# Performance work log

Measured on AMD Instinct MI355X. Metric: run time of the kernel, lower is better.

The kernel has to match this reference:

```python
import jax, jax.numpy as jnp
import numpy as np

B, S, ENC_UNITS, DEC_UNITS, NUM_UNITS = 64, 2048, 512, 512, 512


def setup_inputs() -> dict:
    key = jax.random.key(0)
    k_h, k_eo, k_w1, k_b1, k_w2, k_b2, k_v, k_bv = jax.random.split(key, 8)
    sd = 0.05
    return {
        "H": jax.random.normal(k_h, (B, DEC_UNITS), dtype=jnp.float32),
        "EO": jax.random.normal(k_eo, (B, S, ENC_UNITS), dtype=jnp.float32),
        "W1": jax.random.normal(k_w1, (ENC_UNITS, NUM_UNITS), dtype=jnp.float32) * sd,
        "b1": jnp.zeros((NUM_UNITS,), dtype=jnp.float32),
        "W2": jax.random.normal(k_w2, (DEC_UNITS, NUM_UNITS), dtype=jnp.float32) * sd,
        "b2": jnp.zeros((NUM_UNITS,), dtype=jnp.float32),
        "V": jax.random.normal(k_v, (NUM_UNITS, 1), dtype=jnp.float32) * sd,
        "bv": jnp.zeros((1,), dtype=jnp.float32),
    }


def reference(H, EO, W1, b1, W2, b2, V, bv):
    # H: [B, D], EO: [B, S, E]
    # score = V(tanh(W1(EO) + W2(H)[:, None, :]))  -> [B, S, 1]
    w1_eo = jnp.einsum("bse,eu->bsu", EO, W1) + b1          # [B, S, U]
    w2_h = (H @ W2 + b2)[:, None, :]                          # [B, 1, U]
    score = jnp.tanh(w1_eo + w2_h) @ V + bv                   # [B, S, 1]
    attention_weights = jax.nn.softmax(score, axis=1)         # [B, S, 1]
    context_vector = jnp.sum(attention_weights * EO, axis=1)  # [B, E]
    return context_vector, attention_weights
```

## Files before the change

kernel.cpp:

```cpp
#include <hip/hip_runtime.h>
#include <hip/hip_bf16.h>


typedef __attribute__((ext_vector_type(8))) short bf16x8;
typedef __attribute__((ext_vector_type(4))) float f32x4;

#define NB 64
#define NS 2048
#define NE 512
#define NU 512

#define ASYNC_CP16(gsrc, ldst)                                               \
  __builtin_amdgcn_global_load_lds(                                          \
      (const __attribute__((address_space(1))) unsigned int*)(gsrc),         \
      (__attribute__((address_space(3))) unsigned int*)(ldst), 16, 0, 0)

__device__ __forceinline__ unsigned short f2bf(float f) {
  union { float f; unsigned int u; } x; x.f = f;
  unsigned int u = x.u;
  unsigned int r = (u + 0x7fffu + ((u >> 16) & 1u)) >> 16;
  return (unsigned short)r;
}

__device__ __forceinline__ float bf2f(short s) {
  union { unsigned int u; float f; } x;
  x.u = ((unsigned int)(unsigned short)s) << 16;
  return x.f;
}

__device__ __forceinline__ float tanh_fast(float x) {
  x = fminf(fmaxf(x, -15.f), 15.f);
  float e = __expf(2.f * x);
  return 1.f - 2.f / (e + 1.f);
}

__global__ __launch_bounds__(256) void pack_w1_kernel(
    const float* __restrict__ W1, unsigned short* __restrict__ W1p) {
  int t = blockIdx.x * 256 + threadIdx.x;
  int k = t >> 9, n = t & 511;
  int kt = k >> 5, kr = k & 31;
  int quad = kr >> 3, j = kr & 7;
  int l = (quad << 4) | (n & 15);
  int nt = n >> 4;
  int dst = ((((nt << 4) + kt) * 64 + l) << 3) + j;
  W1p[dst] = f2bf(W1[t]);
}

__global__ __launch_bounds__(512) void compute_c_kernel(
    const float* __restrict__ H, const float* __restrict__ W2,
    const float* __restrict__ b1, const float* __restrict__ b2,
    float* __restrict__ cvec) {
  const int b = blockIdx.x, u = threadIdx.x;
  __shared__ float hs[512];
  hs[u] = H[(b << 9) + u];
  __syncthreads();
  float s = 0.f;
#pragma unroll 8
  for (int d = 0; d < 512; d++) s = fmaf(hs[d], W2[(d << 9) + u], s);
  cvec[(b << 9) + u] = s + b1[u] + b2[u];
}

__global__ __launch_bounds__(256, 2) void scores_ctx_kernel(
    const float* __restrict__ EO, const unsigned short* __restrict__ W1p,
    const float* __restrict__ cvec, const float* __restrict__ V,
    float* __restrict__ scores, float* __restrict__ m_ws,
    float* __restrict__ l_ws, float* __restrict__ ck_ws) {
  __shared__ __align__(16) unsigned short Bs[2][8192];
  __shared__ float cs[512], vs[512];
  __shared__ float sc_l[64], p_l[64];
  __shared__ __align__(16) float cpart[4][512];
  __shared__ float m_sh;

  const int tid = threadIdx.x;
  const int b = blockIdx.x >> 5;
  const int strip = blockIdx.x & 31;
  const int s0 = strip << 6;
  const int lane = tid & 63, wave = tid >> 6;
  const int quad = lane >> 4, col = lane & 15;

  const uint4* W1p4 = (const uint4*)W1p;

#pragma unroll
  for (int i = 0; i < 4; i++)
    ASYNC_CP16(W1p4 + i * 256 + wave * 64 + lane,
               ((char*)&Bs[0][0]) + (i * 256 + wave * 64) * 16);

  cs[tid] = cvec[(b << 9) + tid];
  cs[tid + 256] = cvec[(b << 9) + 256 + tid];
  vs[tid] = V[tid];
  vs[tid + 256] = V[256 + tid];

  bf16x8 afrag[16];
  {
    const float* rp =
        EO + ((size_t)(b * NS + s0 + wave * 16 + col)) * NE + quad * 8;
#pragma unroll
    for (int kt = 0; kt < 16; kt++) {
      float4 x = *(const float4*)(rp + kt * 32);
      float4 y = *(const float4*)(rp + kt * 32 + 4);
      union { short s[8]; bf16x8 v; } u0;
      u0.s[0] = (short)f2bf(x.x); u0.s[1] = (short)f2bf(x.y);
      u0.s[2] = (short)f2bf(x.z); u0.s[3] = (short)f2bf(x.w);
      u0.s[4] = (short)f2bf(y.x); u0.s[5] = (short)f2bf(y.y);
      u0.s[6] = (short)f2bf(y.z); u0.s[7] = (short)f2bf(y.w);
      afrag[kt] = u0.v;
    }
  }

  __syncthreads();

  float sacc[4] = {0.f, 0.f, 0.f, 0.f};

  for (int nt = 0; nt < 32; nt++) {
    const int cur = nt & 1;
    if (nt < 31) {
#pragma unroll
      for (int i = 0; i < 4; i++)
        ASYNC_CP16(W1p4 + (nt + 1) * 1024 + i * 256 + wave * 64 + lane,
                   ((char*)&Bs[cur ^ 1][0]) + (i * 256 + wave * 64) * 16);
    }
    f32x4 acc = {0.f, 0.f, 0.f, 0.f};
    const bf16x8* bp = (const bf16x8*)&Bs[cur][0];
#pragma unroll
    for (int kt = 0; kt < 16; kt++) {
      bf16x8 bfr = bp[kt * 64 + lane];
      acc = __builtin_amdgcn_mfma_f32_16x16x32_bf16(afrag[kt], bfr, acc, 0, 0, 0);
    }
    int u = (nt << 4) + col;
    float cu = cs[u], vu = vs[u];
#pragma unroll
    for (int r = 0; r < 4; r++)
      sacc[r] += tanh_fast(acc[r] + cu) * vu;
    __syncthreads();
  }

#pragma unroll
  for (int m = 1; m < 16; m <<= 1)
#pragma unroll
    for (int r = 0; r < 4; r++)
      sacc[r] += __shfl_xor(sacc[r], m, 64);

  if (col == 0) {
#pragma unroll
    for (int r = 0; r < 4; r++) {
      int row = wave * 16 + quad * 4 + r;
      sc_l[row] = sacc[r];
      scores[(size_t)b * NS + s0 + row] = sacc[r];
    }
  }
  __syncthreads();

  if (wave == 0) {
    float m0 = sc_l[lane];
#pragma unroll
    for (int off = 32; off; off >>= 1) m0 = fmaxf(m0, __shfl_xor(m0, off, 64));
    if (lane == 0) m_sh = m0;
    float p = __expf(sc_l[lane] - m0);
    p_l[lane] = p;
#pragma unroll
    for (int off = 32; off; off >>= 1) p += __shfl_xor(p, off, 64);
    if (lane == 0) {
      m_ws[b * 32 + strip] = m0;
      l_ws[b * 32 + strip] = p;
    }
  }
  __syncthreads();

  const float p0 = p_l[wave * 16 + col];
#pragma unroll
  for (int kt = 0; kt < 16; kt++) {
    float v[8];
#pragma unroll
    for (int j = 0; j < 8; j++) v[j] = p0 * bf2f(afrag[kt][j]);
#pragma unroll
    for (int m = 1; m < 16; m <<= 1)
#pragma unroll
      for (int j = 0; j < 8; j++) v[j] += __shfl_xor(v[j], m, 64);
    if (col == 0) {
      float* dst = &cpart[wave][kt * 32 + quad * 8];
      *(float4*)dst = make_float4(v[0], v[1], v[2], v[3]);
      *(float4*)(dst + 4) = make_float4(v[4], v[5], v[6], v[7]);
    }
  }
  __syncthreads();

  {
    float2 s = {0.f, 0.f};
#pragma unroll
    for (int w = 0; w < 4; w++) {
      float2 t = *(const float2*)&cpart[w][tid * 2];
      s.x += t.x; s.y += t.y;
    }
    *(float2*)&ck_ws[((size_t)(b * 32 + strip)) * 512 + tid * 2] = s;
  }
}

__global__ __launch_bounds__(256) void combine_kernel(
    const float* __restrict__ m_ws, const float* __restrict__ l_ws,
    const float* __restrict__ ck_ws, float* __restrict__ ctx,
    float* __restrict__ w ) {
  const int b = blockIdx.x, tid = threadIdx.x;
  __shared__ float msh[32], lsh[32];
  if (tid < 32) {
    msh[tid] = m_ws[b * 32 + tid];
    lsh[tid] = l_ws[b * 32 + tid];
  }
  __syncthreads();
  float M = msh[0];
#pragma unroll
  for (int k = 1; k < 32; k++) M = fmaxf(M, msh[k]);
  float L = 0.f;
#pragma unroll
  for (int k = 0; k < 32; k++) L += lsh[k] * __expf(msh[k] - M);
  const float invL = 1.f / L;

  float2 acc = {0.f, 0.f};
#pragma unroll
  for (int k = 0; k < 32; k++) {
    float sc = __expf(msh[k] - M);
    float2 t = *(const float2*)&ck_ws[((size_t)(b * 32 + k)) * 512 + tid * 2];
    acc.x += sc * t.x; acc.y += sc * t.y;
  }
  acc.x *= invL; acc.y *= invL;
  *(float2*)&ctx[(b << 9) + tid * 2] = acc;

  float* row = w + (size_t)b * NS;
#pragma unroll
  for (int i = 0; i < 8; i++) {
    float s = row[i * 256 + tid];
    row[i * 256 + tid] = __expf(s - M) * invL;
  }
}

extern "C" void kernel_launch(void* const* d_in, const int* in_sizes, int n_in,
                              void* d_out, int out_size, void* d_ws, size_t ws_size,
                              hipStream_t stream) {
  (void)in_sizes; (void)n_in; (void)out_size; (void)ws_size;
  const float* H  = (const float*)d_in[0];
  const float* EO = (const float*)d_in[1];
  const float* W1 = (const float*)d_in[2];
  const float* b1 = (const float*)d_in[3];
  const float* W2 = (const float*)d_in[4];
  const float* b2 = (const float*)d_in[5];
  const float* V  = (const float*)d_in[6];

  float* out_ctx = (float*)d_out;
  float* out_w   = (float*)d_out + NB * NE;

  char* ws = (char*)d_ws;
  unsigned short* W1p = (unsigned short*)ws;
  float* cvec = (float*)(ws + 512 * 1024);
  float* m_ws = (float*)(ws + 640 * 1024);
  float* l_ws = (float*)(ws + 656 * 1024);
  float* ck_ws = (float*)(ws + 672 * 1024);

  pack_w1_kernel<<<1024, 256, 0, stream>>>(W1, W1p);
  compute_c_kernel<<<NB, 512, 0, stream>>>(H, W2, b1, b2, cvec);
  scores_ctx_kernel<<<2048, 256, 0, stream>>>(EO, W1p, cvec, V, out_w,
                                              m_ws, l_ws, ck_ws);
  combine_kernel<<<NB, 256, 0, stream>>>(m_ws, l_ws, ck_ws, out_ctx, out_w);
}
```

Baseline: 556.5 us.

## Triple-buffer W1 tiles in LDS with explicit vmcnt waits and raw barriers

Grows the LDS buffer for the packed W1 tiles from two to three stages and prefetches two tiles ahead. It replaces `__syncthreads` with `s_waitcnt vmcnt(N)` plus `s_barrier` and `sched_barrier`, so each iteration waits only for the tile it is about to use. The aim is to keep async global-to-LDS copies in flight across the MFMA and tanh work instead of draining every load each iteration. The cost is more LDS per block (about 60KB, still allowing two blocks per CU) and reliance on exact vmcnt counting, which breaks if the order of other outstanding loads changes.

New measurement: 536.7 us. 3.5% less time.

```diff
diff --git a/kernel.cpp b/kernel.cpp
--- a/kernel.cpp
+++ b/kernel.cpp
@@ -14,6 +14,8 @@
   __builtin_amdgcn_global_load_lds(                                          \
       (const __attribute__((address_space(1))) unsigned int*)(gsrc),         \
       (__attribute__((address_space(3))) unsigned int*)(ldst), 16, 0, 0)
+
+#define WAITVM(N) asm volatile("s_waitcnt vmcnt(" #N ")" ::: "memory")
 
 __device__ __forceinline__ unsigned short f2bf(float f) {
   union { float f; unsigned int u; } x; x.f = f;
@@ -65,11 +67,10 @@
     const float* __restrict__ cvec, const float* __restrict__ V,
     float* __restrict__ scores, float* __restrict__ m_ws,
     float* __restrict__ l_ws, float* __restrict__ ck_ws) {
-  __shared__ __align__(16) unsigned short Bs[2][8192];
+  __shared__ __align__(16) unsigned short Bs[3][8192];
   __shared__ float cs[512], vs[512];
   __shared__ float sc_l[64], p_l[64];
   __shared__ __align__(16) float cpart[4][512];
-  __shared__ float m_sh;
 
   const int tid = threadIdx.x;
   const int b = blockIdx.x >> 5;
@@ -109,16 +110,23 @@
 
   __syncthreads();
 
+#pragma unroll
+  for (int tph = 1; tph <= 2; tph++)
+#pragma unroll
+    for (int i = 0; i < 4; i++)
+      ASYNC_CP16(W1p4 + tph * 1024 + i * 256 + wave * 64 + lane,
+                 ((char*)&Bs[tph][0]) + (i * 256 + wave * 64) * 16);
+
   float sacc[4] = {0.f, 0.f, 0.f, 0.f};
-
-  for (int nt = 0; nt < 32; nt++) {
-    const int cur = nt & 1;
-    if (nt < 31) {
-#pragma unroll
-      for (int i = 0; i < 4; i++)
-        ASYNC_CP16(W1p4 + (nt + 1) * 1024 + i * 256 + wave * 64 + lane,
-                   ((char*)&Bs[cur ^ 1][0]) + (i * 256 + wave * 64) * 16);
-    }
+  int cur = 0;
+
+  for (int t = 0; t < 32; t++) {
+    if (t < 30)       WAITVM(8);
+    else if (t == 30) WAITVM(4);
+    else              WAITVM(0);
+    __builtin_amdgcn_s_barrier();
+    __builtin_amdgcn_sched_barrier(0);
+
     f32x4 acc = {0.f, 0.f, 0.f, 0.f};
     const bf16x8* bp = (const bf16x8*)&Bs[cur][0];
 #pragma unroll
@@ -126,12 +134,21 @@
       bf16x8 bfr = bp[kt * 64 + lane];
       acc = __builtin_amdgcn_mfma_f32_16x16x32_bf16(afrag[kt], bfr, acc, 0, 0, 0);
     }
-    int u = (nt << 4) + col;
+    int u = (t << 4) + col;
     float cu = cs[u], vu = vs[u];
 #pragma unroll
     for (int r = 0; r < 4; r++)
       sacc[r] += tanh_fast(acc[r] + cu) * vu;
-    __syncthreads();
+
+    __builtin_amdgcn_sched_barrier(0);
+    __builtin_amdgcn_s_barrier();
+    if (t + 3 < 32) {
+#pragma unroll
+      for (int i = 0; i < 4; i++)
+        ASYNC_CP16(W1p4 + (t + 3) * 1024 + i * 256 + wave * 64 + lane,
+                   ((char*)&Bs[cur][0]) + (i * 256 + wave * 64) * 16);
+    }
+    cur = (cur == 2) ? 0 : cur + 1;
   }
 
 #pragma unroll
@@ -154,7 +171,6 @@
     float m0 = sc_l[lane];
 #pragma unroll
     for (int off = 32; off; off >>= 1) m0 = fmaxf(m0, __shfl_xor(m0, off, 64));
-    if (lane == 0) m_sh = m0;
     float p = __expf(sc_l[lane] - m0);
     p_l[lane] = p;
 #pragma unroll
```
